# Performance work log

Measured on AMD Instinct MI355X. Metric: run time of the kernel, lower is better.

Reference implementation:

```python
import jax, jax.numpy as jnp
import numpy as np

SR = 2  # sr_ratio

def _avgpool2x2(x):
    # x: [B,C,H,W] -> [B,C,H//2,W//2]
    B, C, H, W = x.shape
    return x.reshape(B, C, H // SR, SR, W // SR, SR).mean(axis=(3, 5))

def setup_inputs() -> dict:
    key = jax.random.key(0)
    ks = jax.random.split(key, 6)
    B, C, H, W = 8, 256, 64, 64
    d = C // 8
    sc_qk = 1.0 / np.sqrt(C)
    return {
        "x": jax.random.normal(ks[0], (B, C, H, W), jnp.float32),
        "wq": jax.random.normal(ks[1], (d, C), jnp.float32) * sc_qk,
        "wk": jax.random.normal(ks[2], (d, C), jnp.float32) * sc_qk,
        "wv": jax.random.normal(ks[3], (C, C), jnp.float32) * sc_qk,
        "wo": jax.random.normal(ks[4], (C, C), jnp.float32) * sc_qk,
        "gamma": jax.random.normal(ks[5], (1,), jnp.float32),
    }

def reference(x, wq, wk, wv, wo, gamma):
    B, C, H, W = x.shape
    N = H * W
    d = wq.shape[0]
    # q: conv1x1 then flatten+transpose -> [B, N, d]
    q = jnp.einsum('dc,bchw->bhwd', wq, x).reshape(B, N, d)
    # spatial reduction of K/V source
    x_kv = _avgpool2x2(x)
    Hk, Wk = x_kv.shape[2], x_kv.shape[3]
    Nk = Hk * Wk
    k = jnp.einsum('dc,bchw->bdhw', wk, x_kv).reshape(B, d, Nk)   # [B,d,Nk]
    v = jnp.einsum('oc,bchw->bohw', wv, x_kv).reshape(B, C, Nk)   # [B,C,Nk]
    # attn = softmax(q @ k / sqrt(d)) over Nk
    attn = jax.nn.softmax(jnp.einsum('bnd,bdm->bnm', q, k) / jnp.sqrt(jnp.float32(d)), axis=-1)
    # out = v @ attn^T -> [B,C,N]
    out = jnp.einsum('bcm,bnm->bcn', v, attn).reshape(B, C, H, W)
    out = jnp.einsum('oc,bchw->bohw', wo, out)
    return x + gamma[0] * out
```

## Files before the change

### kernel.cpp

```cpp
#include <hip/hip_runtime.h>

#define BB 8
#define CC 256
#define NN 4096
#define DD 32
#define NK 1024

typedef unsigned short u16;
typedef unsigned int   u32;
typedef __attribute__((ext_vector_type(8))) short bf16x8;
typedef __attribute__((ext_vector_type(4))) float f32x4;

#define MFMA16 __builtin_amdgcn_mfma_f32_16x16x32_bf16

#define OFF_XKVT 0u
#define OFF_WVO  1048576u
#define OFF_WQB  1081344u
#define OFF_WKB  1085440u
#define OFF_QF   1089536u
#define OFF_KF   1613824u
#define OFF_VOF  1744896u

__device__ __forceinline__ u16 f2bf(float f) {
    u32 u = __float_as_uint(f);
    u += 0x7FFFu + ((u >> 16) & 1u);
    return (u16)(u >> 16);
}

__device__ __forceinline__ u32 cvt_pk_bf16(float lo, float hi) {
    u32 r;
    asm("v_cvt_pk_bf16_f32 %0, %1, %2" : "=v"(r) : "v"(lo), "v"(hi));
    return r;
}

__launch_bounds__(256)
__global__ void prepw_kernel(const float* __restrict__ x,
                             const float* __restrict__ wq, const float* __restrict__ wk,
                             const float* __restrict__ wv, const float* __restrict__ wo,
                             u16* __restrict__ xT, u16* __restrict__ xkvT,
                             u16* __restrict__ wqb, u16* __restrict__ wkb,
                             u16* __restrict__ wvob) {
    int t = threadIdx.x;
    if (blockIdx.x < 1024) {
        __shared__ float xl[64 * 132];
        int blk = blockIdx.x;
        int b = blk & 7, rest = blk >> 3, cb = rest & 3, hb = rest >> 2;
        int c0 = cb * 64, n0 = hb * 128;
        const float* xb = x + ((size_t)(b * CC + c0)) * NN + n0;
#pragma unroll
        for (int p = 0; p < 8; ++p) {
            int cr = p * 8 + (t >> 5);
            int ns = (t & 31) * 4;
            *(float4*)&xl[cr * 132 + ns] = *(const float4*)(xb + (size_t)cr * NN + ns);
        }
        __syncthreads();
        {
            int nl = t & 127, ch = t >> 7;
            u16* xp = xT + ((size_t)b * NN + n0 + nl) * CC + c0 + ch * 32;
            u32 wb[16];
#pragma unroll
            for (int j = 0; j < 16; ++j) {
                float a = xl[(ch * 32 + 2 * j) * 132 + nl];
                float c = xl[(ch * 32 + 2 * j + 1) * 132 + nl];
                wb[j] = (u32)f2bf(a) | ((u32)f2bf(c) << 16);
            }
#pragma unroll
            for (int j = 0; j < 4; ++j)
                *(uint4*)(xp + j * 8) = make_uint4(wb[4*j], wb[4*j+1], wb[4*j+2], wb[4*j+3]);
        }
        {
            int wk2 = t & 31, co = t >> 5;
            u32 pw[4];
#pragma unroll
            for (int j = 0; j < 4; ++j) {
                int cl0 = co * 8 + 2 * j;
                float s0 = 0.25f * (xl[cl0*132 + 2*wk2] + xl[cl0*132 + 2*wk2 + 1]
                                  + xl[cl0*132 + 64 + 2*wk2] + xl[cl0*132 + 65 + 2*wk2]);
                int cl1 = cl0 + 1;
                float s1 = 0.25f * (xl[cl1*132 + 2*wk2] + xl[cl1*132 + 2*wk2 + 1]
                                  + xl[cl1*132 + 64 + 2*wk2] + xl[cl1*132 + 65 + 2*wk2]);
                pw[j] = (u32)f2bf(s0) | ((u32)f2bf(s1) << 16);
            }
            u16* kp = xkvT + ((size_t)b * NK + hb * 32 + wk2) * CC + c0 + co * 8;
            *(uint4*)kp = make_uint4(pw[0], pw[1], pw[2], pw[3]);
        }
    } else {
        int o = blockIdx.x - 1024, c = t;
        float acc = 0.f;
#pragma unroll 8
        for (int j = 0; j < CC; ++j)
            acc += wo[o * CC + j] * wv[j * CC + c];
        wvob[o * CC + c] = f2bf(acc);
        int id = o * 256 + t;
        if (id < DD * CC) {
            const float QS = 0.17677669529663687f * 1.4426950408889634f;
            wqb[id] = f2bf(wq[id] * QS);
            wkb[id] = f2bf(wk[id]);
        }
    }
}

__launch_bounds__(256)
__global__ void proj_kernel(const u16* __restrict__ xT, const u16* __restrict__ xkvT,
                            const u16* __restrict__ wqb, const u16* __restrict__ wkb,
                            const u16* __restrict__ wvob,
                            u16* __restrict__ qF, u16* __restrict__ kF,
                            u16* __restrict__ voF) {
    int t = threadIdx.x, w = t >> 6, l = t & 63, l15 = l & 15, lg = l >> 4;
    const f32x4 fz = {0.f, 0.f, 0.f, 0.f};
    if (blockIdx.x < 320) {
        int blk = blockIdx.x;
        const u16 *A, *Bw; u16* outp; int tb4, b;
        if (blk < 256) {
            b = blk & 7;
            int rb = blk >> 3;
            A = xT + ((size_t)b * NN + rb * 128) * CC;
            Bw = wqb;
            outp = qF + (size_t)b * 256 * 512;
            tb4 = rb * 8;
        } else {
            int k2 = blk - 256;
            b = k2 & 7;
            int rb = k2 >> 3;
            A = xkvT + ((size_t)b * NK + rb * 128) * CC;
            Bw = wkb;
            outp = kF + (size_t)b * 64 * 512;
            tb4 = rb * 8;
        }
        const u16* Aw = A + (size_t)(w * 32) * CC;
        f32x4 acc[2][2];
        acc[0][0] = fz; acc[0][1] = fz; acc[1][0] = fz; acc[1][1] = fz;
#pragma unroll
        for (int ks = 0; ks < 8; ++ks) {
            int k0 = ks * 32 + lg * 8;
            bf16x8 a0 = *(const bf16x8*)(Aw + (size_t)l15 * CC + k0);
            bf16x8 a1 = *(const bf16x8*)(Aw + (size_t)(16 + l15) * CC + k0);
            bf16x8 b0 = *(const bf16x8*)(Bw + (size_t)l15 * CC + k0);
            bf16x8 b1 = *(const bf16x8*)(Bw + (size_t)(16 + l15) * CC + k0);
            acc[0][0] = MFMA16(a0, b0, acc[0][0], 0, 0, 0);
            acc[0][1] = MFMA16(a0, b1, acc[0][1], 0, 0, 0);
            acc[1][0] = MFMA16(a1, b0, acc[1][0], 0, 0, 0);
            acc[1][1] = MFMA16(a1, b1, acc[1][1], 0, 0, 0);
        }
#pragma unroll
        for (int i = 0; i < 2; ++i)
#pragma unroll
            for (int jj = 0; jj < 2; ++jj)
#pragma unroll
                for (int r2 = 0; r2 < 4; ++r2) {
                    int tile = tb4 + w * 2 + i;
                    int dhi = jj * 2 + (l15 >> 3);
                    outp[((size_t)tile * 64 + dhi * 16 + lg * 4 + r2) * 8 + (l15 & 7)]
                        = f2bf(acc[i][jj][r2]);
                }
    } else {
        int blk = blockIdx.x - 320;
        int b = blk & 7, r = blk >> 3, ob = r & 3, mb = r >> 2;
        int o0 = ob * 64 + (w & 1) * 32;
        int m0 = mb * 128 + (w >> 1) * 64;
        const u16* ab = wvob + (size_t)o0 * CC;
        const u16* bb = xkvT + ((size_t)b * NK + m0) * CC;
        f32x4 acc[2][4];
#pragma unroll
        for (int i = 0; i < 2; ++i)
#pragma unroll
            for (int j = 0; j < 4; ++j) acc[i][j] = fz;
#pragma unroll
        for (int ks = 0; ks < 8; ++ks) {
            int k0 = ks * 32 + lg * 8;
            bf16x8 a0 = *(const bf16x8*)(ab + (size_t)l15 * CC + k0);
            bf16x8 a1 = *(const bf16x8*)(ab + (size_t)(16 + l15) * CC + k0);
            bf16x8 bv0 = *(const bf16x8*)(bb + (size_t)(l15) * CC + k0);
            bf16x8 bv1 = *(const bf16x8*)(bb + (size_t)(16 + l15) * CC + k0);
            bf16x8 bv2 = *(const bf16x8*)(bb + (size_t)(32 + l15) * CC + k0);
            bf16x8 bv3 = *(const bf16x8*)(bb + (size_t)(48 + l15) * CC + k0);
            acc[0][0] = MFMA16(a0, bv0, acc[0][0], 0, 0, 0);
            acc[0][1] = MFMA16(a0, bv1, acc[0][1], 0, 0, 0);
            acc[0][2] = MFMA16(a0, bv2, acc[0][2], 0, 0, 0);
            acc[0][3] = MFMA16(a0, bv3, acc[0][3], 0, 0, 0);
            acc[1][0] = MFMA16(a1, bv0, acc[1][0], 0, 0, 0);
            acc[1][1] = MFMA16(a1, bv1, acc[1][1], 0, 0, 0);
            acc[1][2] = MFMA16(a1, bv2, acc[1][2], 0, 0, 0);
            acc[1][3] = MFMA16(a1, bv3, acc[1][3], 0, 0, 0);
        }
        u16* vbase = voF + (size_t)b * 32 * 16 * 512;
#pragma unroll
        for (int i = 0; i < 2; ++i)
#pragma unroll
            for (int jj = 0; jj < 4; ++jj)
#pragma unroll
                for (int r2 = 0; r2 < 4; ++r2) {
                    int mt32 = (m0 >> 5) + (jj >> 1);
                    int of   = (o0 >> 4) + i;
                    int mlg  = (jj & 1) * 2 + (l15 >> 3);
                    vbase[(((size_t)mt32 * 16 + of) * 64 + mlg * 16 + lg * 4 + r2) * 8 + (l15 & 7)]
                        = f2bf(acc[i][jj][r2]);
                }
    }
}

__launch_bounds__(512, 4)
__global__ void attn_kernel(const u16* __restrict__ qF, const u16* __restrict__ kF,
                            const u16* __restrict__ voF, const float* __restrict__ x,
                            const float* __restrict__ gamma, float* __restrict__ out) {
    __shared__ __align__(16) u16   p_lds[2][2][64 * 40];
    __shared__ __align__(16) float rs_lds[2][64];

    const int t   = threadIdx.x;
    const int wv  = t >> 6, l = t & 63;
    const int wm  = wv >> 2, wo = wv & 3;
    const int l15 = l & 15, lg = l >> 4;
    const int b   = blockIdx.x & 7;
    const int n0  = (blockIdx.x >> 3) << 6;

    bf16x8 qf = *(const bf16x8*)(qF + ((size_t)(b * 256 + (n0 >> 4) + wo) * 64 + l) * 8);
    const u16* kfp = kF  + ((size_t)(b * 64 + wm * 32) * 64 + l) * 8;
    const u16* vbl = voF + ((size_t)((b * 32 + wm * 16) * 16 + wo * 4) * 64 + l) * 8;

    u16*       pwp = &p_lds[wm][0][(wo * 16 + l15) * 40 + lg * 4];
    const u16* prp = &p_lds[wm][0][l15 * 40 + lg * 8];

    f32x4 acc[4][4];
    const f32x4 fz = {0.f, 0.f, 0.f, 0.f};
#pragma unroll
    for (int j = 0; j < 4; ++j)
#pragma unroll
        for (int of = 0; of < 4; ++of) acc[j][of] = fz;
    float rs = 0.f;

    bf16x8 kf0 = *(const bf16x8*)(kfp);
    bf16x8 kf1 = *(const bf16x8*)(kfp + 512);

#pragma unroll 2
    for (int i = 0; i < 16; ++i) {
        const int buf = i & 1;
        bf16x8 vof[4];
#pragma unroll
        for (int of = 0; of < 4; ++of)
            vof[of] = *(const bf16x8*)(vbl + (size_t)i * 8192 + of * 512);
        f32x4 c0 = MFMA16(kf0, qf, fz, 0, 0, 0);
        f32x4 c1 = MFMA16(kf1, qf, fz, 0, 0, 0);
        float e0 = __builtin_amdgcn_exp2f(c0[0]);
        float e1 = __builtin_amdgcn_exp2f(c0[1]);
        float e2 = __builtin_amdgcn_exp2f(c0[2]);
        float e3 = __builtin_amdgcn_exp2f(c0[3]);
        float e4 = __builtin_amdgcn_exp2f(c1[0]);
        float e5 = __builtin_amdgcn_exp2f(c1[1]);
        float e6 = __builtin_amdgcn_exp2f(c1[2]);
        float e7 = __builtin_amdgcn_exp2f(c1[3]);
        rs += (e0 + e1 + e2 + e3) + (e4 + e5 + e6 + e7);
        uint2 pw0, pw1;
        pw0.x = cvt_pk_bf16(e0, e1);
        pw0.y = cvt_pk_bf16(e2, e3);
        pw1.x = cvt_pk_bf16(e4, e5);
        pw1.y = cvt_pk_bf16(e6, e7);
        u16* pw = pwp + buf * 2560;
        *(uint2*)pw        = pw0;
        *(uint2*)(pw + 16) = pw1;
        asm volatile("s_waitcnt lgkmcnt(0)" ::: "memory");
        __builtin_amdgcn_s_barrier();
        bf16x8 kn0, kn1;
        if (i < 15) {
            kn0 = *(const bf16x8*)(kfp + (size_t)(i * 2 + 2) * 512);
            kn1 = *(const bf16x8*)(kfp + (size_t)(i * 2 + 3) * 512);
        }
        const u16* pr = prp + buf * 2560;
#pragma unroll
        for (int j = 0; j < 4; ++j) {
            bf16x8 pa = *(const bf16x8*)(pr + j * 640);
#pragma unroll
            for (int of = 0; of < 4; ++of)
                acc[j][of] = MFMA16(pa, vof[of], acc[j][of], 0, 0, 0);
        }
        kf0 = kn0; kf1 = kn1;
    }

    rs += __shfl_xor(rs, 16);
    rs += __shfl_xor(rs, 32);
    if (l < 16) rs_lds[wm][wo * 16 + l] = rs;

    __syncthreads();
    float* cbuf = (float*)p_lds;
#pragma unroll
    for (int r = 0; r < 4; ++r) {
        if (wm == 1) {
#pragma unroll
            for (int of = 0; of < 4; ++of)
                *(float4*)&cbuf[((wo * 64 + l) * 16) + of * 4] =
                    make_float4(acc[r][of][0], acc[r][of][1], acc[r][of][2], acc[r][of][3]);
        }
        __syncthreads();
        if (wm == 0) {
#pragma unroll
            for (int of = 0; of < 4; ++of) {
                float4 p = *(const float4*)&cbuf[((wo * 64 + l) * 16) + of * 4];
                acc[r][of][0] += p.x; acc[r][of][1] += p.y;
                acc[r][of][2] += p.z; acc[r][of][3] += p.w;
            }
        }
        __syncthreads();
    }

    if (wm == 0) {
        float g = gamma[0];
#pragma unroll
        for (int j = 0; j < 4; ++j) {
            float r0 = rs_lds[0][j * 16 + lg * 4 + 0] + rs_lds[1][j * 16 + lg * 4 + 0];
            float r1 = rs_lds[0][j * 16 + lg * 4 + 1] + rs_lds[1][j * 16 + lg * 4 + 1];
            float r2 = rs_lds[0][j * 16 + lg * 4 + 2] + rs_lds[1][j * 16 + lg * 4 + 2];
            float r3 = rs_lds[0][j * 16 + lg * 4 + 3] + rs_lds[1][j * 16 + lg * 4 + 3];
            float fa0 = g / r0, fa1 = g / r1, fa2 = g / r2, fa3 = g / r3;
#pragma unroll
            for (int of = 0; of < 4; ++of) {
                size_t base = ((size_t)(b * CC + wo * 64 + of * 16 + l15)) * NN
                            + n0 + j * 16 + lg * 4;
                float4 xv = *(const float4*)(x + base);
                float4 ov;
                ov.x = xv.x + acc[j][of][0] * fa0;
                ov.y = xv.y + acc[j][of][1] * fa1;
                ov.z = xv.z + acc[j][of][2] * fa2;
                ov.w = xv.w + acc[j][of][3] * fa3;
                *(float4*)(out + base) = ov;
            }
        }
    }
}

extern "C" void kernel_launch(void* const* d_in, const int* in_sizes, int n_in,
                              void* d_out, int out_size, void* d_ws, size_t ws_size,
                              hipStream_t stream) {
    const float* x     = (const float*)d_in[0];
    const float* wq    = (const float*)d_in[1];
    const float* wk    = (const float*)d_in[2];
    const float* wv    = (const float*)d_in[3];
    const float* wo    = (const float*)d_in[4];
    const float* gamma = (const float*)d_in[5];
    float* out = (float*)d_out;
    float* ws  = (float*)d_ws;

    u16* xkvT = (u16*)(ws + OFF_XKVT);
    u16* wvob = (u16*)(ws + OFF_WVO);
    u16* wqb  = (u16*)(ws + OFF_WQB);
    u16* wkb  = (u16*)(ws + OFF_WKB);
    u16* qF   = (u16*)(ws + OFF_QF);
    u16* kF   = (u16*)(ws + OFF_KF);
    u16* voF  = (u16*)(ws + OFF_VOF);
    u16* xT   = (u16*)d_out;

    prepw_kernel<<<dim3(1280), dim3(256), 0, stream>>>(x, wq, wk, wv, wo,
                                                       xT, xkvT, wqb, wkb, wvob);
    proj_kernel <<<dim3(576),  dim3(256), 0, stream>>>(xT, xkvT, wqb, wkb, wvob,
                                                       qF, kF, voF);
    attn_kernel <<<dim3(512),  dim3(512), 0, stream>>>(qF, kF, voF, x, gamma, out);
}
```

Measured before the change: 70.29 us.

## Fuse x transpose and avgpool into projection kernel, drop bf16 staging buffers

```diff
diff --git a/kernel.cpp b/kernel.cpp
--- a/kernel.cpp
+++ b/kernel.cpp
@@ -13,13 +13,12 @@
 
 #define MFMA16 __builtin_amdgcn_mfma_f32_16x16x32_bf16
 
-#define OFF_XKVT 0u
-#define OFF_WVO  1048576u
-#define OFF_WQB  1081344u
-#define OFF_WKB  1085440u
-#define OFF_QF   1089536u
-#define OFF_KF   1613824u
-#define OFF_VOF  1744896u
+#define OFF_WVO  0u
+#define OFF_WQB  32768u
+#define OFF_WKB  36864u
+#define OFF_QF   40960u
+#define OFF_KF   565248u
+#define OFF_VOF  696320u
 
 __device__ __forceinline__ u16 f2bf(float f) {
     u32 u = __float_as_uint(f);
@@ -33,169 +32,170 @@
     return r;
 }
 
-__launch_bounds__(256)
-__global__ void prepw_kernel(const float* __restrict__ x,
-                             const float* __restrict__ wq, const float* __restrict__ wk,
+__launch_bounds__(1024)
+__global__ void wprep_kernel(const float* __restrict__ wq, const float* __restrict__ wk,
                              const float* __restrict__ wv, const float* __restrict__ wo,
-                             u16* __restrict__ xT, u16* __restrict__ xkvT,
                              u16* __restrict__ wqb, u16* __restrict__ wkb,
                              u16* __restrict__ wvob) {
-    int t = threadIdx.x;
-    if (blockIdx.x < 1024) {
-        __shared__ float xl[64 * 132];
-        int blk = blockIdx.x;
-        int b = blk & 7, rest = blk >> 3, cb = rest & 3, hb = rest >> 2;
-        int c0 = cb * 64, n0 = hb * 128;
-        const float* xb = x + ((size_t)(b * CC + c0)) * NN + n0;
-#pragma unroll
-        for (int p = 0; p < 8; ++p) {
-            int cr = p * 8 + (t >> 5);
-            int ns = (t & 31) * 4;
-            *(float4*)&xl[cr * 132 + ns] = *(const float4*)(xb + (size_t)cr * NN + ns);
-        }
-        __syncthreads();
-        {
-            int nl = t & 127, ch = t >> 7;
-            u16* xp = xT + ((size_t)b * NN + n0 + nl) * CC + c0 + ch * 32;
-            u32 wb[16];
-#pragma unroll
-            for (int j = 0; j < 16; ++j) {
-                float a = xl[(ch * 32 + 2 * j) * 132 + nl];
-                float c = xl[(ch * 32 + 2 * j + 1) * 132 + nl];
-                wb[j] = (u32)f2bf(a) | ((u32)f2bf(c) << 16);
-            }
-#pragma unroll
-            for (int j = 0; j < 4; ++j)
-                *(uint4*)(xp + j * 8) = make_uint4(wb[4*j], wb[4*j+1], wb[4*j+2], wb[4*j+3]);
-        }
-        {
-            int wk2 = t & 31, co = t >> 5;
-            u32 pw[4];
-#pragma unroll
-            for (int j = 0; j < 4; ++j) {
-                int cl0 = co * 8 + 2 * j;
-                float s0 = 0.25f * (xl[cl0*132 + 2*wk2] + xl[cl0*132 + 2*wk2 + 1]
-                                  + xl[cl0*132 + 64 + 2*wk2] + xl[cl0*132 + 65 + 2*wk2]);
-                int cl1 = cl0 + 1;
-                float s1 = 0.25f * (xl[cl1*132 + 2*wk2] + xl[cl1*132 + 2*wk2 + 1]
-                                  + xl[cl1*132 + 64 + 2*wk2] + xl[cl1*132 + 65 + 2*wk2]);
-                pw[j] = (u32)f2bf(s0) | ((u32)f2bf(s1) << 16);
-            }
-            u16* kp = xkvT + ((size_t)b * NK + hb * 32 + wk2) * CC + c0 + co * 8;
-            *(uint4*)kp = make_uint4(pw[0], pw[1], pw[2], pw[3]);
-        }
-    } else {
-        int o = blockIdx.x - 1024, c = t;
-        float acc = 0.f;
+    __shared__ float part[4][256];
+    int o = blockIdx.x, t = threadIdx.x;
+    int jq = t >> 8, c = t & 255;
+    const float* wvp = wv + (size_t)(jq * 64) * CC + c;
+    const float* wop = wo + o * CC + jq * 64;
+    float acc = 0.f;
 #pragma unroll 8
-        for (int j = 0; j < CC; ++j)
-            acc += wo[o * CC + j] * wv[j * CC + c];
-        wvob[o * CC + c] = f2bf(acc);
-        int id = o * 256 + t;
-        if (id < DD * CC) {
-            const float QS = 0.17677669529663687f * 1.4426950408889634f;
-            wqb[id] = f2bf(wq[id] * QS);
-            wkb[id] = f2bf(wk[id]);
-        }
+    for (int i = 0; i < 64; ++i)
+        acc += wop[i] * wvp[(size_t)i * CC];
+    part[jq][c] = acc;
+    __syncthreads();
+    if (t < 256)
+        wvob[o * CC + t] = f2bf(part[0][t] + part[1][t] + part[2][t] + part[3][t]);
+    if (o < 8) {
+        const float QS = 0.17677669529663687f * 1.4426950408889634f;
+        int id = o * 1024 + t;
+        wqb[id] = f2bf(wq[id] * QS);
+    } else if (o < 16) {
+        int id = (o - 8) * 1024 + t;
+        wkb[id] = f2bf(wk[id]);
     }
 }
 
 __launch_bounds__(256)
-__global__ void proj_kernel(const u16* __restrict__ xT, const u16* __restrict__ xkvT,
+__global__ void proj_kernel(const float* __restrict__ x,
                             const u16* __restrict__ wqb, const u16* __restrict__ wkb,
                             const u16* __restrict__ wvob,
                             u16* __restrict__ qF, u16* __restrict__ kF,
                             u16* __restrict__ voF) {
     int t = threadIdx.x, w = t >> 6, l = t & 63, l15 = l & 15, lg = l >> 4;
     const f32x4 fz = {0.f, 0.f, 0.f, 0.f};
-    if (blockIdx.x < 320) {
-        int blk = blockIdx.x;
-        const u16 *A, *Bw; u16* outp; int tb4, b;
-        if (blk < 256) {
-            b = blk & 7;
-            int rb = blk >> 3;
-            A = xT + ((size_t)b * NN + rb * 128) * CC;
-            Bw = wqb;
-            outp = qF + (size_t)b * 256 * 512;
-            tb4 = rb * 8;
-        } else {
-            int k2 = blk - 256;
-            b = k2 & 7;
-            int rb = k2 >> 3;
-            A = xkvT + ((size_t)b * NK + rb * 128) * CC;
-            Bw = wkb;
-            outp = kF + (size_t)b * 64 * 512;
-            tb4 = rb * 8;
-        }
-        const u16* Aw = A + (size_t)(w * 32) * CC;
+
+    if (blockIdx.x < 256) {
+        __shared__ float xl[64 * 136];
+        int b = blockIdx.x & 7, nb = blockIdx.x >> 3;
+        int n0 = nb * 128;
         f32x4 acc[2][2];
         acc[0][0] = fz; acc[0][1] = fz; acc[1][0] = fz; acc[1][1] = fz;
-#pragma unroll
-        for (int ks = 0; ks < 8; ++ks) {
-            int k0 = ks * 32 + lg * 8;
-            bf16x8 a0 = *(const bf16x8*)(Aw + (size_t)l15 * CC + k0);
-            bf16x8 a1 = *(const bf16x8*)(Aw + (size_t)(16 + l15) * CC + k0);
-            bf16x8 b0 = *(const bf16x8*)(Bw + (size_t)l15 * CC + k0);
-            bf16x8 b1 = *(const bf16x8*)(Bw + (size_t)(16 + l15) * CC + k0);
-            acc[0][0] = MFMA16(a0, b0, acc[0][0], 0, 0, 0);
-            acc[0][1] = MFMA16(a0, b1, acc[0][1], 0, 0, 0);
-            acc[1][0] = MFMA16(a1, b0, acc[1][0], 0, 0, 0);
-            acc[1][1] = MFMA16(a1, b1, acc[1][1], 0, 0, 0);
-        }
+        int cr = t >> 2, seg = (t & 3) * 32;
+        for (int ch = 0; ch < 4; ++ch) {
+            int c0 = ch * 64;
+            const float* xs = x + ((size_t)(b * CC + c0 + cr)) * NN + n0 + seg;
+#pragma unroll
+            for (int p = 0; p < 8; ++p)
+                *(float4*)&xl[cr * 136 + seg + p * 4] = *(const float4*)(xs + p * 4);
+            __syncthreads();
+#pragma unroll
+            for (int ks = 0; ks < 2; ++ks) {
+                int klo = ks * 32 + lg * 8;
+#pragma unroll
+                for (int i = 0; i < 2; ++i) {
+                    int nl = w * 32 + i * 16 + l15;
+                    float f0 = xl[(klo + 0) * 136 + nl];
+                    float f1 = xl[(klo + 1) * 136 + nl];
+                    float f2 = xl[(klo + 2) * 136 + nl];
+                    float f3 = xl[(klo + 3) * 136 + nl];
+                    float f4 = xl[(klo + 4) * 136 + nl];
+                    float f5 = xl[(klo + 5) * 136 + nl];
+                    float f6 = xl[(klo + 6) * 136 + nl];
+                    float f7 = xl[(klo + 7) * 136 + nl];
+                    union { u32 u[4]; bf16x8 v; } cv;
+                    cv.u[0] = cvt_pk_bf16(f0, f1);
+                    cv.u[1] = cvt_pk_bf16(f2, f3);
+                    cv.u[2] = cvt_pk_bf16(f4, f5);
+                    cv.u[3] = cvt_pk_bf16(f6, f7);
+#pragma unroll
+                    for (int dt = 0; dt < 2; ++dt) {
+                        bf16x8 bq = *(const bf16x8*)(wqb + (size_t)(dt * 16 + l15) * CC + c0 + klo);
+                        acc[i][dt] = MFMA16(cv.v, bq, acc[i][dt], 0, 0, 0);
+                    }
+                }
+            }
+            __syncthreads();
+        }
+        u16* outp = qF + (size_t)b * 256 * 512;
 #pragma unroll
         for (int i = 0; i < 2; ++i)
 #pragma unroll
-            for (int jj = 0; jj < 2; ++jj)
+            for (int dt = 0; dt < 2; ++dt)
 #pragma unroll
                 for (int r2 = 0; r2 < 4; ++r2) {
-                    int tile = tb4 + w * 2 + i;
-                    int dhi = jj * 2 + (l15 >> 3);
+                    int tile = nb * 8 + w * 2 + i;
+                    int dhi = dt * 2 + (l15 >> 3);
                     outp[((size_t)tile * 64 + dhi * 16 + lg * 4 + r2) * 8 + (l15 & 7)]
-                        = f2bf(acc[i][jj][r2]);
+                        = f2bf(acc[i][dt][r2]);
                 }
     } else {
-        int blk = blockIdx.x - 320;
-        int b = blk & 7, r = blk >> 3, ob = r & 3, mb = r >> 2;
-        int o0 = ob * 64 + (w & 1) * 32;
-        int m0 = mb * 128 + (w >> 1) * 64;
-        const u16* ab = wvob + (size_t)o0 * CC;
-        const u16* bb = xkvT + ((size_t)b * NK + m0) * CC;
-        f32x4 acc[2][4];
-#pragma unroll
-        for (int i = 0; i < 2; ++i)
-#pragma unroll
-            for (int j = 0; j < 4; ++j) acc[i][j] = fz;
-#pragma unroll
-        for (int ks = 0; ks < 8; ++ks) {
-            int k0 = ks * 32 + lg * 8;
-            bf16x8 a0 = *(const bf16x8*)(ab + (size_t)l15 * CC + k0);
-            bf16x8 a1 = *(const bf16x8*)(ab + (size_t)(16 + l15) * CC + k0);
-            bf16x8 bv0 = *(const bf16x8*)(bb + (size_t)(l15) * CC + k0);
-            bf16x8 bv1 = *(const bf16x8*)(bb + (size_t)(16 + l15) * CC + k0);
-            bf16x8 bv2 = *(const bf16x8*)(bb + (size_t)(32 + l15) * CC + k0);
-            bf16x8 bv3 = *(const bf16x8*)(bb + (size_t)(48 + l15) * CC + k0);
-            acc[0][0] = MFMA16(a0, bv0, acc[0][0], 0, 0, 0);
-            acc[0][1] = MFMA16(a0, bv1, acc[0][1], 0, 0, 0);
-            acc[0][2] = MFMA16(a0, bv2, acc[0][2], 0, 0, 0);
-            acc[0][3] = MFMA16(a0, bv3, acc[0][3], 0, 0, 0);
-            acc[1][0] = MFMA16(a1, bv0, acc[1][0], 0, 0, 0);
-            acc[1][1] = MFMA16(a1, bv1, acc[1][1], 0, 0, 0);
-            acc[1][2] = MFMA16(a1, bv2, acc[1][2], 0, 0, 0);
-            acc[1][3] = MFMA16(a1, bv3, acc[1][3], 0, 0, 0);
-        }
-        u16* vbase = voF + (size_t)b * 32 * 16 * 512;
-#pragma unroll
-        for (int i = 0; i < 2; ++i)
-#pragma unroll
-            for (int jj = 0; jj < 4; ++jj)
-#pragma unroll
-                for (int r2 = 0; r2 < 4; ++r2) {
-                    int mt32 = (m0 >> 5) + (jj >> 1);
-                    int of   = (o0 >> 4) + i;
-                    int mlg  = (jj & 1) * 2 + (l15 >> 3);
-                    vbase[(((size_t)mt32 * 16 + of) * 64 + mlg * 16 + lg * 4 + r2) * 8 + (l15 & 7)]
-                        = f2bf(acc[i][jj][r2]);
-                }
+        __shared__ u16 pl[64 * 42];
+        int blk2 = blockIdx.x - 256;
+        int b = blk2 & 7, hk = blk2 >> 3;
+        f32x4 acck = fz;
+        f32x4 accv[2][4];
+#pragma unroll
+        for (int mt = 0; mt < 2; ++mt)
+#pragma unroll
+            for (int ot = 0; ot < 4; ++ot) accv[mt][ot] = fz;
+
+        int cr = t >> 2, w8 = (t & 3) * 8;
+        for (int ch = 0; ch < 4; ++ch) {
+            int c0 = ch * 64;
+            const float* xs = x + ((size_t)(b * CC + c0 + cr)) * NN + (2 * hk) * 64 + w8 * 2;
+            float4 A0 = *(const float4*)(xs +  0), A1 = *(const float4*)(xs +  4);
+            float4 A2 = *(const float4*)(xs +  8), A3 = *(const float4*)(xs + 12);
+            float4 B0 = *(const float4*)(xs + 64), B1 = *(const float4*)(xs + 68);
+            float4 B2 = *(const float4*)(xs + 72), B3 = *(const float4*)(xs + 76);
+            float p0 = 0.25f * (A0.x + A0.y + B0.x + B0.y);
+            float p1 = 0.25f * (A0.z + A0.w + B0.z + B0.w);
+            float p2 = 0.25f * (A1.x + A1.y + B1.x + B1.y);
+            float p3 = 0.25f * (A1.z + A1.w + B1.z + B1.w);
+            float p4 = 0.25f * (A2.x + A2.y + B2.x + B2.y);
+            float p5 = 0.25f * (A2.z + A2.w + B2.z + B2.w);
+            float p6 = 0.25f * (A3.x + A3.y + B3.x + B3.y);
+            float p7 = 0.25f * (A3.z + A3.w + B3.z + B3.w);
+            u32* pw = (u32*)&pl[cr * 42 + w8];
+            pw[0] = cvt_pk_bf16(p0, p1);
+            pw[1] = cvt_pk_bf16(p2, p3);
+            pw[2] = cvt_pk_bf16(p4, p5);
+            pw[3] = cvt_pk_bf16(p6, p7);
+            __syncthreads();
+#pragma unroll
+            for (int ks = 0; ks < 2; ++ks) {
+                int klo = ks * 32 + lg * 8;
+                bf16x8 pm[2];
+#pragma unroll
+                for (int mt = 0; mt < 2; ++mt) {
+                    union { u16 s[8]; bf16x8 v; } cv;
+#pragma unroll
+                    for (int j = 0; j < 8; ++j)
+                        cv.s[j] = pl[(klo + j) * 42 + mt * 16 + l15];
+                    pm[mt] = cv.v;
+                }
+                {
+                    bf16x8 bk = *(const bf16x8*)(wkb + (size_t)((w & 1) * 16 + l15) * CC + c0 + klo);
+                    acck = MFMA16(pm[w >> 1], bk, acck, 0, 0, 0);
+                }
+#pragma unroll
+                for (int ot = 0; ot < 4; ++ot) {
+                    bf16x8 ao = *(const bf16x8*)(wvob + (size_t)(w * 64 + ot * 16 + l15) * CC + c0 + klo);
+#pragma unroll
+                    for (int mt = 0; mt < 2; ++mt)
+                        accv[mt][ot] = MFMA16(ao, pm[mt], accv[mt][ot], 0, 0, 0);
+                }
+            }
+            __syncthreads();
+        }
+#pragma unroll
+        for (int r2 = 0; r2 < 4; ++r2)
+            kF[((size_t)(b * 64 + hk * 2 + (w >> 1)) * 64
+                + ((w & 1) * 2 + (l15 >> 3)) * 16 + lg * 4 + r2) * 8 + (l15 & 7)]
+                = f2bf(acck[r2]);
+#pragma unroll
+        for (int mt = 0; mt < 2; ++mt)
+#pragma unroll
+            for (int ot = 0; ot < 4; ++ot)
+#pragma unroll
+                for (int r2 = 0; r2 < 4; ++r2)
+                    voF[(((size_t)(b * 32 + hk) * 16 + w * 4 + ot) * 64
+                         + (mt * 2 + (l15 >> 3)) * 16 + lg * 4 + r2) * 8 + (l15 & 7)]
+                        = f2bf(accv[mt][ot][r2]);
     }
 }
 
@@ -265,6 +265,7 @@
             kn1 = *(const bf16x8*)(kfp + (size_t)(i * 2 + 3) * 512);
         }
         const u16* pr = prp + buf * 2560;
+        __builtin_amdgcn_s_setprio(1);
 #pragma unroll
         for (int j = 0; j < 4; ++j) {
             bf16x8 pa = *(const bf16x8*)(pr + j * 640);
@@ -272,6 +273,7 @@
             for (int of = 0; of < 4; ++of)
                 acc[j][of] = MFMA16(pa, vof[of], acc[j][of], 0, 0, 0);
         }
+        __builtin_amdgcn_s_setprio(0);
         kf0 = kn0; kf1 = kn1;
     }
 
@@ -338,18 +340,14 @@
     float* out = (float*)d_out;
     float* ws  = (float*)d_ws;
 
-    u16* xkvT = (u16*)(ws + OFF_XKVT);
     u16* wvob = (u16*)(ws + OFF_WVO);
     u16* wqb  = (u16*)(ws + OFF_WQB);
     u16* wkb  = (u16*)(ws + OFF_WKB);
     u16* qF   = (u16*)(ws + OFF_QF);
     u16* kF   = (u16*)(ws + OFF_KF);
     u16* voF  = (u16*)(ws + OFF_VOF);
-    u16* xT   = (u16*)d_out;
-
-    prepw_kernel<<<dim3(1280), dim3(256), 0, stream>>>(x, wq, wk, wv, wo,
-                                                       xT, xkvT, wqb, wkb, wvob);
-    proj_kernel <<<dim3(576),  dim3(256), 0, stream>>>(xT, xkvT, wqb, wkb, wvob,
-                                                       qF, kF, voF);
-    attn_kernel <<<dim3(512),  dim3(512), 0, stream>>>(qF, kF, voF, x, gamma, out);
-}
+
+    wprep_kernel<<<dim3(256), dim3(1024), 0, stream>>>(wq, wk, wv, wo, wqb, wkb, wvob);
+    proj_kernel <<<dim3(512), dim3(256),  0, stream>>>(x, wqb, wkb, wvob, qF, kF, voF);
+    attn_kernel <<<dim3(512), dim3(512),  0, stream>>>(qF, kF, voF, x, gamma, out);
+}
```

After: 59.59 us. 1.18x faster.
